# Optimization experiments

Hardware: AMD Instinct MI355X
Metric: run time of the kernel (lower is better)

Reference implementation:

```python
import jax, jax.numpy as jnp
import numpy as np

H = 4          # num attention heads
LRELU = 0.2    # DGL GATConv leaky-relu slope
N_GT, N_AG = 100000, 20000
E_GT, E_COMM = 640000, 320000
D_GT, D_AG = 32, 64
VIS, COMM, MSG, OUT = 64, 128, 64, 5
NUM_COMM_STEPS = 2


def _leaky(x):
    return jnp.where(x >= 0, x, LRELU * x)


def gat(feat_src, feat_dst, w_src, w_dst, a_l, a_r, bias, src, dst, n_dst, dh):
    """Bipartite DGL GATConv: residual=Identity (in_dst == H*dh), activation=ReLU."""
    fs = (feat_src @ w_src).reshape(-1, H, dh)   # [Ns,H,dh]
    fd = (feat_dst @ w_dst).reshape(-1, H, dh)   # [Nd,H,dh]
    el = (fs * a_l[None]).sum(-1)                # [Ns,H]
    er = (fd * a_r[None]).sum(-1)                # [Nd,H]
    e = _leaky(el[src] + er[dst])                # [E,H]
    emax = jax.ops.segment_max(e, dst, num_segments=n_dst)
    ex = jnp.exp(e - emax[dst])
    denom = jax.ops.segment_sum(ex, dst, num_segments=n_dst)
    a = ex / denom[dst]                          # edge softmax over in-edges
    rst = jax.ops.segment_sum(fs[src] * a[..., None], dst, num_segments=n_dst)
    rst = rst + feat_dst.reshape(n_dst, H, dh)   # identity residual
    rst = rst + bias.reshape(1, H, dh)
    return jax.nn.relu(rst).reshape(n_dst, H * dh)


def gru(x, h, w_ih, w_hh, b_ih, b_hh):
    gi = x @ w_ih + b_ih
    gh = h @ w_hh + b_hh
    i_r, i_z, i_n = jnp.split(gi, 3, axis=1)
    h_r, h_z, h_n = jnp.split(gh, 3, axis=1)
    r = jax.nn.sigmoid(i_r + h_r)
    zg = jax.nn.sigmoid(i_z + h_z)
    n = jnp.tanh(i_n + r * h_n)
    return (1.0 - zg) * n + zg * h


def setup_inputs() -> dict:
    key = jax.random.key(0)
    ks = jax.random.split(key, 32)
    def w(k, shp):
        return (jax.random.normal(k, shp, dtype=jnp.float32) / np.sqrt(shp[0])).astype(jnp.float32)
    dh1, dh2 = VIS // H, COMM // H
    inp = {
        'feat_gt': jax.random.normal(ks[0], (N_GT, D_GT), dtype=jnp.float32),
        'feat_agent': jax.random.normal(ks[1], (N_AG, D_AG), dtype=jnp.float32),
        'z': jax.random.normal(ks[2], (N_AG, COMM), dtype=jnp.float32),
        'gt_src': jax.random.randint(ks[3], (E_GT,), 0, N_GT, dtype=jnp.int32),
        'gt_dst': jax.random.randint(ks[4], (E_GT,), 0, N_AG, dtype=jnp.int32),
        'comm_src': jax.random.randint(ks[5], (E_COMM,), 0, N_AG, dtype=jnp.int32),
        'comm_dst': jax.random.randint(ks[6], (E_COMM,), 0, N_AG, dtype=jnp.int32),
        # vis1 GATConv (gt->agent), out 64 = 4 heads x 16
        'w1_src': w(ks[7], (D_GT, VIS)), 'w1_dst': w(ks[8], (D_AG, VIS)),
        'a1_l': w(ks[9], (H, dh1)), 'a1_r': w(ks[10], (H, dh1)),
        'b1': jnp.zeros((VIS,), jnp.float32),
        'w2_src': w(ks[11], (D_GT, COMM)), 'w2_dst': w(ks[12], (VIS + D_AG, COMM)),
        'a2_l': w(ks[13], (H, dh2)), 'a2_r': w(ks[14], (H, dh2)),
        'b2': jnp.zeros((COMM,), jnp.float32),
        # comm f_enc: mlp([128,128,64]) with ReLU everywhere
        'enc_w1': w(ks[15], (COMM, 128)), 'enc_b1': jnp.zeros((128,), jnp.float32),
        'enc_w2': w(ks[16], (128, MSG)), 'enc_b2': jnp.zeros((MSG,), jnp.float32),
        # GRUCell(in=COMM+MSG=192, hidden=COMM=128), stored [in, 3*hidden]
        'gru_w_ih': w(ks[17], (COMM + MSG, 3 * COMM)),
        'gru_w_hh': w(ks[18], (COMM, 3 * COMM)),
        'gru_b_ih': jnp.zeros((3 * COMM,), jnp.float32),
        'gru_b_hh': jnp.zeros((3 * COMM,), jnp.float32),
        # f_out
        'out_w': w(ks[19], (COMM, OUT)), 'out_b': jnp.zeros((OUT,), jnp.float32),
    }
    return inp


def _forward(feat_gt, feat_agent, z, gt_src, gt_dst, comm_src, comm_dst,
             w1_src, w1_dst, a1_l, a1_r, b1,
             w2_src, w2_dst, a2_l, a2_r, b2,
             enc_w1, enc_b1, enc_w2, enc_b2,
             gru_w_ih, gru_w_hh, gru_b_ih, gru_b_hh,
             out_w, out_b):
    n_ag = feat_agent.shape[0]
    h_vis1 = gat(feat_gt, feat_agent, w1_src, w1_dst, a1_l, a1_r, b1,
                 gt_src, gt_dst, n_ag, VIS // H)
    dst2 = jnp.concatenate([h_vis1, feat_agent], axis=1)
    h = gat(feat_gt, dst2, w2_src, w2_dst, a2_l, a2_r, b2,
            gt_src, gt_dst, n_ag, COMM // H)
    deg = jax.ops.segment_sum(jnp.ones_like(comm_dst, dtype=jnp.float32),
                              comm_dst, num_segments=n_ag)
    denom = jnp.maximum(deg, 1.0)[:, None]
    zz = z
    for _ in range(NUM_COMM_STEPS):
        m = jax.nn.relu(jax.nn.relu(h @ enc_w1 + enc_b1) @ enc_w2 + enc_b2)  # per-node f_enc
        y = jax.ops.segment_sum(m[comm_src], comm_dst, num_segments=n_ag) / denom  # mailbox mean
        h = gru(jnp.concatenate([h, y], axis=1), zz, gru_w_ih, gru_w_hh, gru_b_ih, gru_b_hh)
        zz = h
    h_out = h @ out_w + out_b
    return h_out, zz


def reference(feat_gt, feat_agent, z, gt_src, gt_dst, comm_src, comm_dst,
              w1_src, w1_dst, a1_l, a1_r, b1,
              w2_src, w2_dst, a2_l, a2_r, b2,
              enc_w1, enc_b1, enc_w2, enc_b2,
              gru_w_ih, gru_w_hh, gru_b_ih, gru_b_hh,
              out_w, out_b):
    return _forward(feat_gt, feat_agent, z, gt_src, gt_dst, comm_src, comm_dst,
                    w1_src, w1_dst, a1_l, a1_r, b1,
                    w2_src, w2_dst, a2_l, a2_r, b2,
                    enc_w1, enc_b1, enc_w2, enc_b2,
                    gru_w_ih, gru_w_hh, gru_b_ih, gru_b_hh,
                    out_w, out_b)
```

## Files before the change

### kernel.cpp

```cpp
#include <hip/hip_runtime.h>
#include <math.h>

#define NHEAD 4
#define LRELU_S 0.2f
constexpr int N_GT = 100000, N_AG = 20000;
constexpr int E_GT = 640000, E_COMM = 320000;
constexpr int OUTD = 5;
constexpr int NBLK_SC = (N_AG + 255) / 256;

constexpr long O_CNTP_GT = 0;
constexpr long O_CNTP_CM = 320000;
constexpr long O_FSB1    = 0;
constexpr long O_FSB2    = 3200000;
constexpr long O_EL1     = 12800000;
constexpr long O_EL2     = 13200000;
constexpr long O_RST1    = 13600000;
constexpr long O_ER1     = 14880000;
constexpr long O_ER2     = 14960000;
constexpr long O_RST2    = 17600000;
constexpr long O_DINV    = 20160000;
constexpr long O_OFFS_GT = 20180000;
constexpr long O_SRT_GT  = 20200004;
constexpr long O_OFFS_CM = 20840004;
constexpr long O_SRT_CM  = 20860008;
constexpr long O_PART    = 21180008;
constexpr long O_V       = 21220008;
constexpr long O_WB      = 21300000;
constexpr long O_RANK_GT = 21500000;
constexpr long O_RANK_CM = 22140000;
constexpr long O_T1 = 7680000;
constexpr long O_M  = 10240000;
constexpr long O_Y  = 15360000;

constexpr long WB_FS  = 0;
constexpr long WB_E1  = 6144;
constexpr long WB_E2  = 22528;
constexpr long WB_RZ  = 30720;
constexpr long WB_GIN = 112640;
constexpr long WB_GHN = 137216;

using bf8      = __attribute__((ext_vector_type(8))) short;
using f32x4v   = __attribute__((ext_vector_type(4))) float;
using ushort8v = __attribute__((ext_vector_type(8))) unsigned short;

__device__ __forceinline__ unsigned short f2bf(float x) {
    unsigned u = __float_as_uint(x);
    u += 0x7FFFu + ((u >> 16) & 1u);
    return (unsigned short)(u >> 16);
}
__device__ __forceinline__ float bf2f(unsigned short u) {
    return __uint_as_float(((unsigned)u) << 16);
}

__global__ void fill_u32_k(unsigned* __restrict__ p, unsigned v, int n) {
    int i = blockIdx.x * blockDim.x + threadIdx.x;
    if (i < n) p[i] = v;
}

__global__ void count_rank_k(const int* __restrict__ gdst, unsigned* __restrict__ gcnt,
                             unsigned* __restrict__ grank,
                             const int* __restrict__ cdst, unsigned* __restrict__ ccnt,
                             unsigned* __restrict__ crank) {
    int i = blockIdx.x * blockDim.x + threadIdx.x;
    if (i < E_GT) {
        grank[i] = atomicAdd(gcnt + (long)gdst[i] * 16, 1u);
    } else if (i < E_GT + E_COMM) {
        int j = i - E_GT;
        crank[j] = atomicAdd(ccnt + (long)cdst[j] * 16, 1u);
    }
}

__global__ __launch_bounds__(256) void bscan_k(const unsigned* __restrict__ cnt_gt,
                                               const unsigned* __restrict__ cnt_cm,
                                               unsigned* __restrict__ offs_gt,
                                               unsigned* __restrict__ offs_cm,
                                               unsigned* __restrict__ partials,
                                               float* __restrict__ dinv) {
    __shared__ unsigned sh[256];
    const int g = (blockIdx.x >= NBLK_SC) ? 1 : 0;
    const int b = blockIdx.x - g * NBLK_SC;
    const int t = threadIdx.x;
    const int i = b * 256 + t;
    const unsigned* cnt = g ? cnt_cm : cnt_gt;
    unsigned c = (i < N_AG) ? cnt[(long)i * 16] : 0u;
    if (g && i < N_AG) dinv[i] = 1.0f / fmaxf((float)c, 1.0f);
    sh[t] = c;
    __syncthreads();
    for (int off = 1; off < 256; off <<= 1) {
        unsigned v = (t >= off) ? sh[t - off] : 0u;
        __syncthreads();
        sh[t] += v;
        __syncthreads();
    }
    unsigned* offs = g ? offs_cm : offs_gt;
    if (i < N_AG) offs[i] = sh[t] - c;
    if (t == 255) partials[blockIdx.x] = sh[255];
}

__global__ __launch_bounds__(256) void padd_k(unsigned* __restrict__ offs_gt,
                                              unsigned* __restrict__ offs_cm,
                                              const unsigned* __restrict__ partials) {
    __shared__ unsigned sh[128];
    const int g = (blockIdx.x >= NBLK_SC) ? 1 : 0;
    const int b = blockIdx.x - g * NBLK_SC;
    const int t = threadIdx.x;
    if (t < 128) sh[t] = (t < (unsigned)b) ? partials[g * NBLK_SC + t] : 0u;
    __syncthreads();
    for (int off = 64; off >= 1; off >>= 1) {
        if (t < (unsigned)off) sh[t] += sh[t + off];
        __syncthreads();
    }
    const unsigned pre = sh[0];
    unsigned* offs = g ? offs_cm : offs_gt;
    const int i = b * 256 + t;
    if (i < N_AG) offs[i] += pre;
    if (blockIdx.x == NBLK_SC - 1 && t == 0) offs_gt[N_AG] = E_GT;
    if (blockIdx.x == 2 * NBLK_SC - 1 && t == 0) offs_cm[N_AG] = E_COMM;
}

__global__ void place2_k(const int* __restrict__ gsrc, const int* __restrict__ gdst,
                         const unsigned* __restrict__ grank, const unsigned* __restrict__ goffs,
                         unsigned* __restrict__ gsort,
                         const int* __restrict__ csrc, const int* __restrict__ cdst,
                         const unsigned* __restrict__ crank, const unsigned* __restrict__ coffs,
                         unsigned* __restrict__ csort) {
    int i = blockIdx.x * blockDim.x + threadIdx.x;
    if (i < E_GT) {
        gsort[goffs[gdst[i]] + grank[i]] = (unsigned)gsrc[i];
    } else if (i < E_GT + E_COMM) {
        int j = i - E_GT;
        csort[coffs[cdst[j]] + crank[j]] = (unsigned)csrc[j];
    }
}

__global__ void wconv_all_k(const float* __restrict__ w1, const float* __restrict__ w2,
                            const float* __restrict__ e1, const float* __restrict__ e2,
                            const float* __restrict__ gih, const float* __restrict__ ghh,
                            unsigned short* __restrict__ wb) {
    int i = blockIdx.x * blockDim.x + threadIdx.x;
    if (i >= 153600) return;
    float val;
    if (i < 2048)        { long l = i;          long n = l / 32,  k = l % 32;  val = w1[k * 64 + n]; }
    else if (i < 6144)   { long l = i - 2048;   long n = l / 32,  k = l % 32;  val = w2[k * 128 + n]; }
    else if (i < 22528)  { long l = i - 6144;   long n = l / 128, k = l % 128; val = e1[k * 128 + n]; }
    else if (i < 30720)  { long l = i - 22528;  long n = l / 128, k = l % 128; val = e2[k * 64 + n]; }
    else if (i < 112640) { long l = i - 30720;  long n = l / 320, k = l % 320;
                           val = (k < 192) ? gih[k * 384 + n] : ghh[(k - 192) * 384 + n]; }
    else if (i < 137216) { long l = i - 112640; long n = l / 192, k = l % 192; val = gih[k * 384 + 256 + n]; }
    else                 { long l = i - 137216; long n = l / 128, k = l % 128; val = ghh[k * 384 + 256 + n]; }
    wb[i] = f2bf(val);
}

__global__ void make_v_all_k(const float* __restrict__ w1s, const float* __restrict__ a1l,
                             const float* __restrict__ w1d, const float* __restrict__ a1r,
                             const float* __restrict__ w2s, const float* __restrict__ a2l,
                             const float* __restrict__ w2d, const float* __restrict__ a2r,
                             float* __restrict__ v) {
    int i = blockIdx.x * blockDim.x + threadIdx.x;
    if (i >= 1024) return;
    const float *w, *a; int dh, local;
    if (i < 128)      { w = w1s; a = a1l; dh = 16; local = i; }
    else if (i < 384) { w = w1d; a = a1r; dh = 16; local = i - 128; }
    else if (i < 512) { w = w2s; a = a2l; dh = 32; local = i - 384; }
    else              { w = w2d; a = a2r; dh = 32; local = i - 512; }
    int k = local >> 2, h = local & 3;
    float s = 0.f;
    for (int j = 0; j < dh; ++j) s += w[k * (4 * dh) + h * dh + j] * a[h * dh + j];
    v[i] = s;
}

__global__ void rowvec_all_k(const float* __restrict__ fgt, const float* __restrict__ fag,
                             const float* __restrict__ v1, const float* __restrict__ v2,
                             const float* __restrict__ vr1,
                             float* __restrict__ el1, float* __restrict__ el2,
                             float* __restrict__ er1) {
    int i = blockIdx.x * blockDim.x + threadIdx.x;
    if (i < N_GT) {
        float a[8] = {};
        const float* fp = fgt + (long)i * 32;
        for (int k = 0; k < 32; ++k) {
            float x = fp[k];
#pragma unroll
            for (int j = 0; j < 4; ++j) a[j] += x * v1[4 * k + j];
#pragma unroll
            for (int j = 0; j < 4; ++j) a[4 + j] += x * v2[4 * k + j];
        }
        *reinterpret_cast<float4*>(el1 + 4l * i) = {a[0], a[1], a[2], a[3]};
        *reinterpret_cast<float4*>(el2 + 4l * i) = {a[4], a[5], a[6], a[7]};
    } else if (i < N_GT + N_AG) {
        int r = i - N_GT;
        float a0 = 0, a1 = 0, a2 = 0, a3 = 0;
        const float* fp = fag + (long)r * 64;
        for (int k = 0; k < 64; ++k) {
            float x = fp[k];
            a0 += x * vr1[4 * k]; a1 += x * vr1[4 * k + 1];
            a2 += x * vr1[4 * k + 2]; a3 += x * vr1[4 * k + 3];
        }
        *reinterpret_cast<float4*>(er1 + 4l * r) = {a0, a1, a2, a3};
    }
}

template <int ACT, int OB>
__global__ __launch_bounds__(256) void mgemm_k(const float* __restrict__ A,
                                               const float* __restrict__ A2, int K1,
                                               const unsigned short* __restrict__ Bt,
                                               const float* __restrict__ bias,
                                               void* __restrict__ Cv,
                                               int M, int N, int K) {
    __shared__ unsigned short As[64][40];
    __shared__ unsigned short Bs[64][40];
    const int tid = threadIdx.x;
    const int lane = tid & 63, wv = tid >> 6;
    const int wm = wv & 1, wn = wv >> 1;
    const int quad = lane >> 4, l16 = lane & 15;
    const int m0 = blockIdx.y * 64, n0 = blockIdx.x * 64;
    const int K2 = K - K1;
    f32x4v acc[2][2] = {};
    const int rA = tid >> 3, cA = (tid & 7) * 4;
    const int rB = tid >> 2, cB = (tid & 3) * 8;

    for (int k0 = 0; k0 < K; k0 += 32) {
#pragma unroll
        for (int half = 0; half < 2; ++half) {
            const int r = rA + half * 32;
            const int row = m0 + r;
            const int kg = k0 + cA;
            float4 v = {0.f, 0.f, 0.f, 0.f};
            if (row < M) {
                v = (kg < K1) ? *reinterpret_cast<const float4*>(A + (long)row * K1 + kg)
                              : *reinterpret_cast<const float4*>(A2 + (long)row * K2 + (kg - K1));
            }
            ushort4 b;
            b.x = f2bf(v.x); b.y = f2bf(v.y); b.z = f2bf(v.z); b.w = f2bf(v.w);
            *reinterpret_cast<ushort4*>(&As[r][cA]) = b;
        }
        *reinterpret_cast<ushort8v*>(&Bs[rB][cB]) =
            *reinterpret_cast<const ushort8v*>(Bt + (long)(n0 + rB) * K + k0 + cB);
        __syncthreads();

        const bf8 a0 = *reinterpret_cast<const bf8*>(&As[wm * 32 + l16][quad * 8]);
        const bf8 a1 = *reinterpret_cast<const bf8*>(&As[wm * 32 + 16 + l16][quad * 8]);
        const bf8 b0 = *reinterpret_cast<const bf8*>(&Bs[wn * 32 + l16][quad * 8]);
        const bf8 b1 = *reinterpret_cast<const bf8*>(&Bs[wn * 32 + 16 + l16][quad * 8]);
        acc[0][0] = __builtin_amdgcn_mfma_f32_16x16x32_bf16(a0, b0, acc[0][0], 0, 0, 0);
        acc[0][1] = __builtin_amdgcn_mfma_f32_16x16x32_bf16(a0, b1, acc[0][1], 0, 0, 0);
        acc[1][0] = __builtin_amdgcn_mfma_f32_16x16x32_bf16(a1, b0, acc[1][0], 0, 0, 0);
        acc[1][1] = __builtin_amdgcn_mfma_f32_16x16x32_bf16(a1, b1, acc[1][1], 0, 0, 0);
        __syncthreads();
    }

#pragma unroll
    for (int mt = 0; mt < 2; ++mt)
#pragma unroll
        for (int nt = 0; nt < 2; ++nt)
#pragma unroll
            for (int r = 0; r < 4; ++r) {
                const int row = m0 + wm * 32 + mt * 16 + quad * 4 + r;
                const int col = n0 + wn * 32 + nt * 16 + l16;
                if (row < M) {
                    float v = acc[mt][nt][r];
                    if (bias) v += bias[col];
                    if (ACT) v = fmaxf(v, 0.f);
                    if (OB) ((unsigned short*)Cv)[(long)row * N + col] = f2bf(v);
                    else    ((float*)Cv)[(long)row * N + col] = v;
                }
            }
}

__global__ __launch_bounds__(512) void grugemm_k(
    const float* __restrict__ h, const float* __restrict__ y, const float* __restrict__ zz,
    const unsigned short* __restrict__ wrz, const unsigned short* __restrict__ wgin,
    const unsigned short* __restrict__ wghn,
    const float* __restrict__ b_ih, const float* __restrict__ b_hh,
    float* __restrict__ hout, int M)
{
    __shared__ unsigned short As[32][328];
    const int tid = threadIdx.x;
    const int lane = tid & 63, w = tid >> 6;
    const int quad = lane >> 4, l16 = lane & 15;
    const int m0 = blockIdx.x * 32;
#pragma unroll
    for (int it = 0; it < 5; ++it) {
        int idx = tid + it * 512;
        int row = idx / 80, cc = (idx - row * 80) * 4;
        int grow = m0 + row;
        float4 v = {0.f, 0.f, 0.f, 0.f};
        if (grow < M) {
            if (cc < 128)      v = *reinterpret_cast<const float4*>(h + (long)grow * 128 + cc);
            else if (cc < 192) v = *reinterpret_cast<const float4*>(y + (long)grow * 64 + (cc - 128));
            else               v = *reinterpret_cast<const float4*>(zz + (long)grow * 128 + (cc - 192));
        }
        ushort4 b;
        b.x = f2bf(v.x); b.y = f2bf(v.y); b.z = f2bf(v.z); b.w = f2bf(v.w);
        *reinterpret_cast<ushort4*>(&As[row][cc]) = b;
    }
    __syncthreads();

    f32x4v aR[2] = {}, aZ[2] = {}, aI[2] = {}, aH[2] = {};
    const int j0 = w * 16;
    const unsigned short* pR = wrz + (long)(j0 + l16) * 320 + quad * 8;
    const unsigned short* pZ = wrz + (long)(128 + j0 + l16) * 320 + quad * 8;
#pragma unroll
    for (int half = 0; half < 2; ++half) {
        bf8 bR[5], bZ[5];
#pragma unroll
        for (int i = 0; i < 5; ++i) {
            const int k0 = half * 160 + i * 32;
            bR[i] = *reinterpret_cast<const bf8*>(pR + k0);
            bZ[i] = *reinterpret_cast<const bf8*>(pZ + k0);
        }
#pragma unroll
        for (int i = 0; i < 5; ++i) {
            const int k0 = half * 160 + i * 32;
            const bf8 a0 = *reinterpret_cast<const bf8*>(&As[l16][k0 + quad * 8]);
            const bf8 a1 = *reinterpret_cast<const bf8*>(&As[16 + l16][k0 + quad * 8]);
            aR[0] = __builtin_amdgcn_mfma_f32_16x16x32_bf16(a0, bR[i], aR[0], 0, 0, 0);
            aR[1] = __builtin_amdgcn_mfma_f32_16x16x32_bf16(a1, bR[i], aR[1], 0, 0, 0);
            aZ[0] = __builtin_amdgcn_mfma_f32_16x16x32_bf16(a0, bZ[i], aZ[0], 0, 0, 0);
            aZ[1] = __builtin_amdgcn_mfma_f32_16x16x32_bf16(a1, bZ[i], aZ[1], 0, 0, 0);
        }
    }
    {
        const unsigned short* pI = wgin + (long)(j0 + l16) * 192 + quad * 8;
        bf8 bI[6];
#pragma unroll
        for (int i = 0; i < 6; ++i) bI[i] = *reinterpret_cast<const bf8*>(pI + i * 32);
#pragma unroll
        for (int i = 0; i < 6; ++i) {
            const int k0 = i * 32;
            const bf8 a0 = *reinterpret_cast<const bf8*>(&As[l16][k0 + quad * 8]);
            const bf8 a1 = *reinterpret_cast<const bf8*>(&As[16 + l16][k0 + quad * 8]);
            aI[0] = __builtin_amdgcn_mfma_f32_16x16x32_bf16(a0, bI[i], aI[0], 0, 0, 0);
            aI[1] = __builtin_amdgcn_mfma_f32_16x16x32_bf16(a1, bI[i], aI[1], 0, 0, 0);
        }
    }
    {
        const unsigned short* pH = wghn + (long)(j0 + l16) * 128 + quad * 8;
        bf8 bH[4];
#pragma unroll
        for (int i = 0; i < 4; ++i) bH[i] = *reinterpret_cast<const bf8*>(pH + i * 32);
#pragma unroll
        for (int i = 0; i < 4; ++i) {
            const int k0 = 192 + i * 32;
            const bf8 a0 = *reinterpret_cast<const bf8*>(&As[l16][k0 + quad * 8]);
            const bf8 a1 = *reinterpret_cast<const bf8*>(&As[16 + l16][k0 + quad * 8]);
            aH[0] = __builtin_amdgcn_mfma_f32_16x16x32_bf16(a0, bH[i], aH[0], 0, 0, 0);
            aH[1] = __builtin_amdgcn_mfma_f32_16x16x32_bf16(a1, bH[i], aH[1], 0, 0, 0);
        }
    }
    const int j = j0 + l16;
#pragma unroll
    for (int mt = 0; mt < 2; ++mt)
#pragma unroll
        for (int r = 0; r < 4; ++r) {
            const int row = m0 + mt * 16 + quad * 4 + r;
            if (row >= M) continue;
            const float rr = 1.f / (1.f + __expf(-(aR[mt][r] + b_ih[j] + b_hh[j])));
            const float zg = 1.f / (1.f + __expf(-(aZ[mt][r] + b_ih[128 + j] + b_hh[128 + j])));
            const float nn = tanhf(aI[mt][r] + b_ih[256 + j] + rr * (aH[mt][r] + b_hh[256 + j]));
            const float hp = zz[(long)row * 128 + j];
            hout[(long)row * 128 + j] = (1.f - zg) * nn + zg * hp;
        }
}

__global__ __launch_bounds__(256) void fs_gemm_k(const float* __restrict__ A,
                                                 const unsigned short* __restrict__ Btc,
                                                 unsigned short* __restrict__ fsb1,
                                                 unsigned short* __restrict__ fsb2, int M) {
    __shared__ unsigned short As[64][40];
    __shared__ unsigned short Bs[64][40];
    const int tid = threadIdx.x;
    const int lane = tid & 63, wv = tid >> 6;
    const int wm = wv & 1, wn = wv >> 1;
    const int quad = lane >> 4, l16 = lane & 15;
    const int m0 = blockIdx.y * 64, n0 = blockIdx.x * 64;
    f32x4v acc[2][2] = {};
    const int rA = tid >> 3, cA = (tid & 7) * 4;
    const int rB = tid >> 2, cB = (tid & 3) * 8;

#pragma unroll
    for (int half = 0; half < 2; ++half) {
        const int r = rA + half * 32;
        const int row = m0 + r;
        float4 v = {0.f, 0.f, 0.f, 0.f};
        if (row < M) v = *reinterpret_cast<const float4*>(A + (long)row * 32 + cA);
        ushort4 b;
        b.x = f2bf(v.x); b.y = f2bf(v.y); b.z = f2bf(v.z); b.w = f2bf(v.w);
        *reinterpret_cast<ushort4*>(&As[r][cA]) = b;
    }
    *reinterpret_cast<ushort8v*>(&Bs[rB][cB]) =
        *reinterpret_cast<const ushort8v*>(Btc + (long)(n0 + rB) * 32 + cB);
    __syncthreads();

    const bf8 a0 = *reinterpret_cast<const bf8*>(&As[wm * 32 + l16][quad * 8]);
    const bf8 a1 = *reinterpret_cast<const bf8*>(&As[wm * 32 + 16 + l16][quad * 8]);
    const bf8 b0 = *reinterpret_cast<const bf8*>(&Bs[wn * 32 + l16][quad * 8]);
    const bf8 b1 = *reinterpret_cast<const bf8*>(&Bs[wn * 32 + 16 + l16][quad * 8]);
    acc[0][0] = __builtin_amdgcn_mfma_f32_16x16x32_bf16(a0, b0, acc[0][0], 0, 0, 0);
    acc[0][1] = __builtin_amdgcn_mfma_f32_16x16x32_bf16(a0, b1, acc[0][1], 0, 0, 0);
    acc[1][0] = __builtin_amdgcn_mfma_f32_16x16x32_bf16(a1, b0, acc[1][0], 0, 0, 0);
    acc[1][1] = __builtin_amdgcn_mfma_f32_16x16x32_bf16(a1, b1, acc[1][1], 0, 0, 0);

#pragma unroll
    for (int mt = 0; mt < 2; ++mt)
#pragma unroll
        for (int nt = 0; nt < 2; ++nt)
#pragma unroll
            for (int r = 0; r < 4; ++r) {
                const int row = m0 + wm * 32 + mt * 16 + quad * 4 + r;
                const int col = n0 + wn * 32 + nt * 16 + l16;
                if (row < M) {
                    unsigned short v16 = f2bf(acc[mt][nt][r]);
                    if (col < 64) fsb1[(long)row * 64 + col] = v16;
                    else          fsb2[(long)row * 128 + (col - 64)] = v16;
                }
            }
}

template <int CH, int ER2>
__global__ __launch_bounds__(256) void gat_fused_k(
    const unsigned* __restrict__ offs, const unsigned* __restrict__ ssrc,
    const float* __restrict__ el, const float* __restrict__ er,
    const unsigned short* __restrict__ fsb,
    const float* __restrict__ res0, const float* __restrict__ res1,
    const float* __restrict__ bias, float* __restrict__ out, int n_dst, unsigned nsrc,
    const float* __restrict__ vr2, float* __restrict__ er2)
{
    constexpr int CPL = CH / 64;
    const int wid = threadIdx.x >> 6;
    const int lane = threadIdx.x & 63;
    const int d = blockIdx.x * 4 + wid;
    if (d >= n_dst) return;
    const int h = lane >> 4, ei = lane & 15;
    const float er_h = er[4l * d + h];
    const unsigned beg = offs[d], end = offs[d + 1];
    const int c0 = lane * CPL;
    const unsigned smax = nsrc - 1u;
    float m = -INFINITY, s = 0.f, acc0 = 0.f, acc1 = 0.f;

    for (unsigned base = beg; base < end; base += 16) {
        const unsigned na = min(16u, end - base);
        unsigned sv = ssrc[base + ((unsigned)ei < na ? (unsigned)ei : 0u)];
        sv = min(sv, smax);
        unsigned fw[16];
#pragma unroll
        for (int j = 0; j < 16; ++j) {
            const unsigned sj = (unsigned)__shfl((int)sv, j);
            if (CPL == 2) fw[j] = *reinterpret_cast<const unsigned*>(fsb + (long)sj * CH + c0);
            else          fw[j] = fsb[(long)sj * CH + c0];
        }
        float xv = -INFINITY;
        if ((unsigned)ei < na) {
            float x = el[4l * sv + h] + er_h;
            xv = (x >= 0.f) ? x : LRELU_S * x;
        }
        float cm = xv;
#pragma unroll
        for (int off = 1; off < 16; off <<= 1) cm = fmaxf(cm, __shfl_xor(cm, off));
        const float mn = fmaxf(m, cm);
        const float corr = __expf(m - mn);
        const float p = __expf(xv - mn);
        float ps = p;
#pragma unroll
        for (int off = 1; off < 16; off <<= 1) ps += __shfl_xor(ps, off);
        s = s * corr + ps;
        acc0 *= corr; acc1 *= corr;
        m = mn;
#pragma unroll
        for (int j = 0; j < 16; ++j) {
            const float pj = __shfl(p, (h << 4) | j);
            if (CPL == 2) {
                acc0 += pj * __uint_as_float((fw[j] & 0xFFFFu) << 16);
                acc1 += pj * __uint_as_float((fw[j] >> 16) << 16);
            } else {
                acc0 += pj * bf2f((unsigned short)fw[j]);
            }
        }
    }
    const float inv = (s > 0.f) ? 1.f / s : 0.f;
    if (CPL == 1) {
        const float r = res0[(long)d * 64 + c0];
        const float o = fmaxf(acc0 * inv + r + bias[c0], 0.f);
        out[(long)d * 64 + c0] = o;
        if (ER2) {
            float e[4];
#pragma unroll
            for (int hh = 0; hh < 4; ++hh)
                e[hh] = o * vr2[c0 * 4 + hh] + r * vr2[(64 + c0) * 4 + hh];
#pragma unroll
            for (int off = 1; off < 64; off <<= 1) {
#pragma unroll
                for (int hh = 0; hh < 4; ++hh) e[hh] += __shfl_xor(e[hh], off);
            }
            if (lane == 0)
                *reinterpret_cast<float4*>(er2 + 4l * d) = {e[0], e[1], e[2], e[3]};
        }
    } else {
        float2 r = (c0 < 64) ? *reinterpret_cast<const float2*>(res0 + (long)d * 64 + c0)
                             : *reinterpret_cast<const float2*>(res1 + (long)d * 64 + (c0 - 64));
        float2 o;
        o.x = fmaxf(acc0 * inv + r.x + bias[c0], 0.f);
        o.y = fmaxf(acc1 * inv + r.y + bias[c0 + 1], 0.f);
        *reinterpret_cast<float2*>(out + (long)d * 128 + c0) = o;
    }
}

__global__ __launch_bounds__(256) void comm_gather_k(const unsigned* __restrict__ offs,
                                                     const unsigned* __restrict__ ssrc,
                                                     const unsigned short* __restrict__ mb,
                                                     const float* __restrict__ dinv,
                                                     float* __restrict__ y, int n) {
    const int wid = threadIdx.x >> 6;
    const int lane = threadIdx.x & 63;
    const int d = blockIdx.x * 4 + wid;
    if (d >= n) return;
    const unsigned beg = offs[d], end = offs[d + 1];
    const int ei = lane & 15;
    const unsigned smax = (unsigned)n - 1u;
    float acc = 0.f;
    for (unsigned base = beg; base < end; base += 16) {
        const unsigned na = min(16u, end - base);
        unsigned sv = ssrc[base + ((unsigned)ei < na ? (unsigned)ei : 0u)];
        sv = min(sv, smax);
        unsigned short fw[16];
#pragma unroll
        for (int j = 0; j < 16; ++j) {
            const unsigned sj = (unsigned)__shfl((int)sv, j);
            fw[j] = mb[(long)sj * 64 + lane];
        }
#pragma unroll
        for (int j = 0; j < 16; ++j)
            if ((unsigned)j < na) acc += bf2f(fw[j]);
    }
    y[(long)d * 64 + lane] = acc * dinv[d];
}

__global__ void outcopy_k(const float* __restrict__ h, const float* __restrict__ w,
                          const float* __restrict__ b, float* __restrict__ out) {
    int i = blockIdx.x * blockDim.x + threadIdx.x;
    if (i >= N_AG * 128) return;
    out[(long)N_AG * OUTD + i] = h[i];
    if (i < N_AG) {
        float acc[OUTD];
#pragma unroll
        for (int j = 0; j < OUTD; ++j) acc[j] = b[j];
        for (int k = 0; k < 128; ++k) {
            float v = h[(long)i * 128 + k];
#pragma unroll
            for (int j = 0; j < OUTD; ++j) acc[j] += v * w[k * OUTD + j];
        }
#pragma unroll
        for (int j = 0; j < OUTD; ++j) out[(long)i * OUTD + j] = acc[j];
    }
}

extern "C" void kernel_launch(void* const* d_in, const int* in_sizes, int n_in,
                              void* d_out, int out_size, void* d_ws, size_t ws_size,
                              hipStream_t stream) {
    const float* feat_gt    = (const float*)d_in[0];
    const float* feat_agent = (const float*)d_in[1];
    const float* z_in       = (const float*)d_in[2];
    const int*   gt_src     = (const int*)d_in[3];
    const int*   gt_dst     = (const int*)d_in[4];
    const int*   comm_src   = (const int*)d_in[5];
    const int*   comm_dst   = (const int*)d_in[6];
    const float* w1_src = (const float*)d_in[7];
    const float* w1_dst = (const float*)d_in[8];
    const float* a1_l   = (const float*)d_in[9];
    const float* a1_r   = (const float*)d_in[10];
    const float* b1     = (const float*)d_in[11];
    const float* w2_src = (const float*)d_in[12];
    const float* w2_dst = (const float*)d_in[13];
    const float* a2_l   = (const float*)d_in[14];
    const float* a2_r   = (const float*)d_in[15];
    const float* b2     = (const float*)d_in[16];
    const float* enc_w1 = (const float*)d_in[17];
    const float* enc_b1 = (const float*)d_in[18];
    const float* enc_w2 = (const float*)d_in[19];
    const float* enc_b2 = (const float*)d_in[20];
    const float* gw_ih  = (const float*)d_in[21];
    const float* gw_hh  = (const float*)d_in[22];
    const float* gb_ih  = (const float*)d_in[23];
    const float* gb_hh  = (const float*)d_in[24];
    const float* out_w  = (const float*)d_in[25];
    const float* out_b  = (const float*)d_in[26];

    float* ws = (float*)d_ws;
    unsigned* wsu = (unsigned*)d_ws;
    unsigned short* wb = (unsigned short*)(ws + O_WB);
    float* out = (float*)d_out;

    auto blk = [](long n) { return dim3((unsigned)((n + 255) / 256)); };
    const dim3 T(256);

    fill_u32_k<<<blk(640000), T, 0, stream>>>(wsu + O_CNTP_GT, 0u, 640000);
    count_rank_k<<<blk(E_GT + E_COMM), T, 0, stream>>>(gt_dst, wsu + O_CNTP_GT, wsu + O_RANK_GT,
                                                       comm_dst, wsu + O_CNTP_CM, wsu + O_RANK_CM);
    bscan_k<<<2 * NBLK_SC, T, 0, stream>>>(wsu + O_CNTP_GT, wsu + O_CNTP_CM,
                                           wsu + O_OFFS_GT, wsu + O_OFFS_CM,
                                           wsu + O_PART, ws + O_DINV);
    padd_k<<<2 * NBLK_SC, T, 0, stream>>>(wsu + O_OFFS_GT, wsu + O_OFFS_CM, wsu + O_PART);
    place2_k<<<blk(E_GT + E_COMM), T, 0, stream>>>(gt_src, gt_dst, wsu + O_RANK_GT, wsu + O_OFFS_GT, wsu + O_SRT_GT,
                                                   comm_src, comm_dst, wsu + O_RANK_CM, wsu + O_OFFS_CM, wsu + O_SRT_CM);

    wconv_all_k<<<blk(153600), T, 0, stream>>>(w1_src, w2_src, enc_w1, enc_w2, gw_ih, gw_hh, wb);
    make_v_all_k<<<4, 256, 0, stream>>>(w1_src, a1_l, w1_dst, a1_r, w2_src, a2_l, w2_dst, a2_r, ws + O_V);
    float* VL1 = ws + O_V, *VR1 = ws + O_V + 128, *VL2 = ws + O_V + 384, *VR2 = ws + O_V + 512;
    rowvec_all_k<<<blk(N_GT + N_AG), T, 0, stream>>>(feat_gt, feat_agent, VL1, VL2, VR1,
                                                     ws + O_EL1, ws + O_EL2, ws + O_ER1);

    const int MB_GT = (N_GT + 63) / 64, MB_AG = (N_AG + 63) / 64;
    unsigned short* fsb1 = (unsigned short*)(ws + O_FSB1);
    unsigned short* fsb2 = (unsigned short*)(ws + O_FSB2);

    fs_gemm_k<<<dim3(3, MB_GT), T, 0, stream>>>(feat_gt, wb + WB_FS, fsb1, fsb2, N_GT);

    gat_fused_k<64, 1><<<dim3((N_AG + 3) / 4), T, 0, stream>>>(wsu + O_OFFS_GT, wsu + O_SRT_GT,
        ws + O_EL1, ws + O_ER1, fsb1, feat_agent, nullptr, b1, ws + O_RST1, N_AG, N_GT,
        VR2, ws + O_ER2);

    gat_fused_k<128, 0><<<dim3((N_AG + 3) / 4), T, 0, stream>>>(wsu + O_OFFS_GT, wsu + O_SRT_GT,
        ws + O_EL2, ws + O_ER2, fsb2, ws + O_RST1, feat_agent, b2, ws + O_RST2, N_AG, N_GT,
        nullptr, nullptr);

    float* h = ws + O_RST2;
    unsigned short* mb = (unsigned short*)(ws + O_M);
    for (int step = 0; step < 2; ++step) {
        const float* zz = (step == 0) ? z_in : h;
        mgemm_k<1, 0><<<dim3(2, MB_AG), T, 0, stream>>>(h, nullptr, 128, wb + WB_E1, enc_b1, ws + O_T1, N_AG, 128, 128);
        mgemm_k<1, 1><<<dim3(1, MB_AG), T, 0, stream>>>(ws + O_T1, nullptr, 128, wb + WB_E2, enc_b2, mb, N_AG, 64, 128);
        comm_gather_k<<<dim3((N_AG + 3) / 4), T, 0, stream>>>(wsu + O_OFFS_CM, wsu + O_SRT_CM,
            mb, ws + O_DINV, ws + O_Y, N_AG);
        grugemm_k<<<dim3((N_AG + 31) / 32), dim3(512), 0, stream>>>(h, ws + O_Y, zz,
            wb + WB_RZ, wb + WB_GIN, wb + WB_GHN, gb_ih, gb_hh, h, N_AG);
    }

    outcopy_k<<<blk((long)N_AG * 128), T, 0, stream>>>(h, out_w, out_b, out);
}
```

Before: 414.2 us.

## Fuse the two encoder MLP GEMMs into one kernel with an LDS-resident intermediate

Replaces the two generic mgemm_k launches for the per-node encoder MLP with one fused kernel. Each 512-thread block loads 32 rows of h into LDS as bf16 and computes the first layer with MFMA, keeping weight fragments in registers. The ReLU output stays in LDS as bf16, and the second layer then writes the bf16 message. This removes the fp32 intermediate's global round trip and one launch per communication step. The trade-off is that the intermediate is now rounded to bf16, and half the waves sit idle during the second layer.

```diff
diff --git a/kernel.cpp b/kernel.cpp
--- a/kernel.cpp
+++ b/kernel.cpp
@@ -28,7 +28,6 @@
 constexpr long O_WB      = 21300000;
 constexpr long O_RANK_GT = 21500000;
 constexpr long O_RANK_CM = 22140000;
-constexpr long O_T1 = 7680000;
 constexpr long O_M  = 10240000;
 constexpr long O_Y  = 15360000;
 
@@ -200,71 +199,81 @@
     }
 }
 
-template <int ACT, int OB>
-__global__ __launch_bounds__(256) void mgemm_k(const float* __restrict__ A,
-                                               const float* __restrict__ A2, int K1,
-                                               const unsigned short* __restrict__ Bt,
-                                               const float* __restrict__ bias,
-                                               void* __restrict__ Cv,
-                                               int M, int N, int K) {
-    __shared__ unsigned short As[64][40];
-    __shared__ unsigned short Bs[64][40];
+__global__ __launch_bounds__(512) void enc_fused_k(
+    const float* __restrict__ h,
+    const unsigned short* __restrict__ we1,
+    const unsigned short* __restrict__ we2,
+    const float* __restrict__ eb1, const float* __restrict__ eb2,
+    unsigned short* __restrict__ mb, int M)
+{
+    __shared__ unsigned short As[32][136];
+    __shared__ unsigned short Ts[32][136];
     const int tid = threadIdx.x;
-    const int lane = tid & 63, wv = tid >> 6;
-    const int wm = wv & 1, wn = wv >> 1;
+    const int lane = tid & 63, w = tid >> 6;
     const int quad = lane >> 4, l16 = lane & 15;
-    const int m0 = blockIdx.y * 64, n0 = blockIdx.x * 64;
-    const int K2 = K - K1;
-    f32x4v acc[2][2] = {};
-    const int rA = tid >> 3, cA = (tid & 7) * 4;
-    const int rB = tid >> 2, cB = (tid & 3) * 8;
-
-    for (int k0 = 0; k0 < K; k0 += 32) {
-#pragma unroll
-        for (int half = 0; half < 2; ++half) {
-            const int r = rA + half * 32;
-            const int row = m0 + r;
-            const int kg = k0 + cA;
-            float4 v = {0.f, 0.f, 0.f, 0.f};
-            if (row < M) {
-                v = (kg < K1) ? *reinterpret_cast<const float4*>(A + (long)row * K1 + kg)
-                              : *reinterpret_cast<const float4*>(A2 + (long)row * K2 + (kg - K1));
+    const int m0 = blockIdx.x * 32;
+#pragma unroll
+    for (int it = 0; it < 2; ++it) {
+        int idx = tid + it * 512;
+        int row = idx >> 5, cc = (idx & 31) * 4;
+        int grow = m0 + row;
+        float4 v = {0.f, 0.f, 0.f, 0.f};
+        if (grow < M) v = *reinterpret_cast<const float4*>(h + (long)grow * 128 + cc);
+        ushort4 b;
+        b.x = f2bf(v.x); b.y = f2bf(v.y); b.z = f2bf(v.z); b.w = f2bf(v.w);
+        *reinterpret_cast<ushort4*>(&As[row][cc]) = b;
+    }
+    __syncthreads();
+    {
+        const int j0 = w * 16;
+        const unsigned short* p = we1 + (long)(j0 + l16) * 128 + quad * 8;
+        bf8 bw[4];
+#pragma unroll
+        for (int i = 0; i < 4; ++i) bw[i] = *reinterpret_cast<const bf8*>(p + i * 32);
+        f32x4v acc[2] = {};
+#pragma unroll
+        for (int i = 0; i < 4; ++i) {
+            const int k0 = i * 32;
+            const bf8 a0 = *reinterpret_cast<const bf8*>(&As[l16][k0 + quad * 8]);
+            const bf8 a1 = *reinterpret_cast<const bf8*>(&As[16 + l16][k0 + quad * 8]);
+            acc[0] = __builtin_amdgcn_mfma_f32_16x16x32_bf16(a0, bw[i], acc[0], 0, 0, 0);
+            acc[1] = __builtin_amdgcn_mfma_f32_16x16x32_bf16(a1, bw[i], acc[1], 0, 0, 0);
+        }
+        const int j = j0 + l16;
+        const float bj = eb1[j];
+#pragma unroll
+        for (int mt = 0; mt < 2; ++mt)
+#pragma unroll
+            for (int r = 0; r < 4; ++r)
+                Ts[mt * 16 + quad * 4 + r][j] = f2bf(fmaxf(acc[mt][r] + bj, 0.f));
+    }
+    __syncthreads();
+    if (w < 4) {
+        const int j0 = w * 16;
+        const unsigned short* p = we2 + (long)(j0 + l16) * 128 + quad * 8;
+        bf8 bw[4];
+#pragma unroll
+        for (int i = 0; i < 4; ++i) bw[i] = *reinterpret_cast<const bf8*>(p + i * 32);
+        f32x4v acc[2] = {};
+#pragma unroll
+        for (int i = 0; i < 4; ++i) {
+            const int k0 = i * 32;
+            const bf8 a0 = *reinterpret_cast<const bf8*>(&Ts[l16][k0 + quad * 8]);
+            const bf8 a1 = *reinterpret_cast<const bf8*>(&Ts[16 + l16][k0 + quad * 8]);
+            acc[0] = __builtin_amdgcn_mfma_f32_16x16x32_bf16(a0, bw[i], acc[0], 0, 0, 0);
+            acc[1] = __builtin_amdgcn_mfma_f32_16x16x32_bf16(a1, bw[i], acc[1], 0, 0, 0);
+        }
+        const int j = j0 + l16;
+        const float bj = eb2[j];
+#pragma unroll
+        for (int mt = 0; mt < 2; ++mt)
+#pragma unroll
+            for (int r = 0; r < 4; ++r) {
+                const int row = m0 + mt * 16 + quad * 4 + r;
+                if (row < M)
+                    mb[(long)row * 64 + j] = f2bf(fmaxf(acc[mt][r] + bj, 0.f));
             }
-            ushort4 b;
-            b.x = f2bf(v.x); b.y = f2bf(v.y); b.z = f2bf(v.z); b.w = f2bf(v.w);
-            *reinterpret_cast<ushort4*>(&As[r][cA]) = b;
-        }
-        *reinterpret_cast<ushort8v*>(&Bs[rB][cB]) =
-            *reinterpret_cast<const ushort8v*>(Bt + (long)(n0 + rB) * K + k0 + cB);
-        __syncthreads();
-
-        const bf8 a0 = *reinterpret_cast<const bf8*>(&As[wm * 32 + l16][quad * 8]);
-        const bf8 a1 = *reinterpret_cast<const bf8*>(&As[wm * 32 + 16 + l16][quad * 8]);
-        const bf8 b0 = *reinterpret_cast<const bf8*>(&Bs[wn * 32 + l16][quad * 8]);
-        const bf8 b1 = *reinterpret_cast<const bf8*>(&Bs[wn * 32 + 16 + l16][quad * 8]);
-        acc[0][0] = __builtin_amdgcn_mfma_f32_16x16x32_bf16(a0, b0, acc[0][0], 0, 0, 0);
-        acc[0][1] = __builtin_amdgcn_mfma_f32_16x16x32_bf16(a0, b1, acc[0][1], 0, 0, 0);
-        acc[1][0] = __builtin_amdgcn_mfma_f32_16x16x32_bf16(a1, b0, acc[1][0], 0, 0, 0);
-        acc[1][1] = __builtin_amdgcn_mfma_f32_16x16x32_bf16(a1, b1, acc[1][1], 0, 0, 0);
-        __syncthreads();
-    }
-
-#pragma unroll
-    for (int mt = 0; mt < 2; ++mt)
-#pragma unroll
-        for (int nt = 0; nt < 2; ++nt)
-#pragma unroll
-            for (int r = 0; r < 4; ++r) {
-                const int row = m0 + wm * 32 + mt * 16 + quad * 4 + r;
-                const int col = n0 + wn * 32 + nt * 16 + l16;
-                if (row < M) {
-                    float v = acc[mt][nt][r];
-                    if (bias) v += bias[col];
-                    if (ACT) v = fmaxf(v, 0.f);
-                    if (OB) ((unsigned short*)Cv)[(long)row * N + col] = f2bf(v);
-                    else    ((float*)Cv)[(long)row * N + col] = v;
-                }
-            }
+    }
 }
 
 __global__ __launch_bounds__(512) void grugemm_k(
@@ -609,7 +618,7 @@
     rowvec_all_k<<<blk(N_GT + N_AG), T, 0, stream>>>(feat_gt, feat_agent, VL1, VL2, VR1,
                                                      ws + O_EL1, ws + O_EL2, ws + O_ER1);
 
-    const int MB_GT = (N_GT + 63) / 64, MB_AG = (N_AG + 63) / 64;
+    const int MB_GT = (N_GT + 63) / 64;
     unsigned short* fsb1 = (unsigned short*)(ws + O_FSB1);
     unsigned short* fsb2 = (unsigned short*)(ws + O_FSB2);
 
@@ -627,8 +636,8 @@
     unsigned short* mb = (unsigned short*)(ws + O_M);
     for (int step = 0; step < 2; ++step) {
         const float* zz = (step == 0) ? z_in : h;
-        mgemm_k<1, 0><<<dim3(2, MB_AG), T, 0, stream>>>(h, nullptr, 128, wb + WB_E1, enc_b1, ws + O_T1, N_AG, 128, 128);
-        mgemm_k<1, 1><<<dim3(1, MB_AG), T, 0, stream>>>(ws + O_T1, nullptr, 128, wb + WB_E2, enc_b2, mb, N_AG, 64, 128);
+        enc_fused_k<<<dim3((N_AG + 31) / 32), dim3(512), 0, stream>>>(
+            h, wb + WB_E1, wb + WB_E2, enc_b1, enc_b2, mb, N_AG);
         comm_gather_k<<<dim3((N_AG + 3) / 4), T, 0, stream>>>(wsu + O_OFFS_CM, wsu + O_SRT_CM,
             mb, ws + O_DINV, ws + O_Y, N_AG);
         grugemm_k<<<dim3((N_AG + 31) / 32), dim3(512), 0, stream>>>(h, ws + O_Y, zz,
```

Result: faster. 395.3 us (-4.6%).
